# Kernel tuning notes

Measured on AMD Instinct MI355X. Metric: run time of the kernel, lower is better.

Reference implementation:

```python
import jax, jax.numpy as jnp
import numpy as np

B, N, T, CIN = 16, 400, 12, 2
HID, H, D = 256, 8, 32
P, EMB, TOPK, K = 3, 10, 16, 3


def _conv1d(x, w, b, dil):
    # x: (BN, C, T), w: (O, I, K); causal (left) padding like F.pad((pad,0))
    pad = (K - 1) * dil
    y = jax.lax.conv_general_dilated(x, w, (1,), [(pad, 0)], rhs_dilation=(dil,),
                                     dimension_numbers=('NCH', 'OIH', 'NCH'))
    return y + b[None, :, None]


def _ln(x, g, b):
    m = x.mean(-1, keepdims=True)
    v = x.var(-1, keepdims=True)
    return (x - m) / jnp.sqrt(v + 1e-5) * g + b


def setup_inputs() -> dict:
    key = jax.random.key(0)
    kit = iter(jax.random.split(key, 64))

    def g(shape, s=0.05):
        return jax.random.normal(next(kit), shape, jnp.float32) * s

    # fixed graph: ring with 8 neighbors + self loop -> L = 9*N edges
    idx = np.arange(N)
    offs = np.array([-4, -3, -2, -1, 0, 1, 2, 3, 4])
    recv = np.repeat(idx, offs.size)
    send = (recv + np.tile(offs, N)) % N
    L = recv.size

    inp = {
        'x': g((B, N, T, CIN), 1.0),
        'edge_feat': g((B, L, 2), 1.0),
        'fixed_edge_index': jnp.asarray(np.stack([recv, send]).astype(np.int32)),
        # GTCN layer 0 (dilation 1): gate/filter/skip convs + LayerNorm
        'wg0': g((HID, CIN, K)), 'bg0': jnp.zeros((HID,), jnp.float32),
        'wf0': g((HID, CIN, K)), 'bf0': jnp.zeros((HID,), jnp.float32),
        'ws0': g((HID, CIN, K)), 'bs0': jnp.zeros((HID,), jnp.float32),
        'ln0g': jnp.ones((HID,), jnp.float32), 'ln0b': jnp.zeros((HID,), jnp.float32),
        # GTCN layer 1 (dilation 2)
        'wg1': g((HID, HID, K)), 'bg1': jnp.zeros((HID,), jnp.float32),
        'wf1': g((HID, HID, K)), 'bf1': jnp.zeros((HID,), jnp.float32),
        'ws1': g((HID, HID, K)), 'bs1': jnp.zeros((HID,), jnp.float32),
        'ln1g': jnp.ones((HID,), jnp.float32), 'ln1b': jnp.zeros((HID,), jnp.float32),
        'wsk': g((CIN, HID)), 'bsk': jnp.zeros((HID,), jnp.float32),
        # sparse GAT on fixed physical graph (with 2-dim edge features)
        'sWq': g((HID, HID)), 'sWk': g((HID, HID)), 'sWv': g((HID, HID)),
        'sWe': g((2, HID)),
        'saq': g((H, D)), 'sak': g((H, D)), 'sae': g((H, D)),
        # dense GAT on adaptive adjacency
        'dWq': g((HID, HID)), 'dWk': g((HID, HID)), 'dWv': g((HID, HID)),
        'daq': g((H, D)), 'dak': g((H, D)),
        'E1': g((N, EMB), 0.5), 'E2': g((N, EMB), 0.5),
        # gated fusion
        'fW1': g((HID, HID)), 'fb1': jnp.zeros((HID,), jnp.float32),
        'fW2': g((HID, HID)), 'fb2': jnp.zeros((HID,), jnp.float32),
        'fW3': g((HID, HID)), 'fb3': jnp.zeros((HID,), jnp.float32),
        # prediction head
        'Wo': g((HID, P)), 'bo': jnp.zeros((P,), jnp.float32),
    }
    return inp


def reference(x, edge_feat,
              wg0, bg0, wf0, bf0, ws0, bs0, ln0g, ln0b,
              wg1, bg1, wf1, bf1, ws1, bs1, ln1g, ln1b, wsk, bsk,
              sWq, sWk, sWv, sWe, saq, sak, sae,
              dWq, dWk, dWv, daq, dak, E1, E2,
              fW1, fb1, fW2, fb2, fW3, fb3, Wo, bo,
              fixed_edge_index):
    Bb, Nn, Tt, _ = x.shape
    # ---- GTCN (gated temporal conv stack with residual skip) ----
    res = x @ wsk + bsk                                   # (B,N,T,HID)
    xc = x.reshape(Bb * Nn, Tt, -1).transpose(0, 2, 1)    # (BN,C,T)
    for (wg, bg, wf, bf, ws, bs, lg, lb), dil in (
            ((wg0, bg0, wf0, bf0, ws0, bs0, ln0g, ln0b), 1),
            ((wg1, bg1, wf1, bf1, ws1, bs1, ln1g, ln1b), 2)):
        gate = jax.nn.sigmoid(_conv1d(xc, wg, bg, dil))
        y = gate * _conv1d(xc, wf, bf, dil) + (1 - gate) * _conv1d(xc, ws, bs, dil)
        y = jax.nn.relu(_ln(y.transpose(0, 2, 1), lg, lb))  # (BN,T,HID)
        xc = y.transpose(0, 2, 1)
    h = xc.transpose(0, 2, 1).reshape(Bb, Nn, Tt, HID) + res
    hl = h[:, :, -1, :]                                   # (B,N,HID) last step

    # ---- sparse GAT on fixed physical graph (edge features) ----
    recv, send = fixed_edge_index[0], fixed_edge_index[1]
    q = (hl @ sWq).reshape(Bb, Nn, H, D)
    k = (hl @ sWk).reshape(Bb, Nn, H, D)
    v = (hl @ sWv).reshape(Bb, Nn, H, D)
    e = (edge_feat @ sWe).reshape(Bb, -1, H, D)
    s = (q[:, recv] * saq).sum(-1) + (k[:, send] * sak).sum(-1) + (e * sae).sum(-1)
    s = jax.nn.leaky_relu(s, 0.2)                         # (B,L,H)
    mx = jnp.full((Bb, Nn, H), -jnp.inf, s.dtype).at[:, recv].max(s)
    ex = jnp.exp(s - mx[:, recv])
    den = jnp.zeros((Bb, Nn, H), s.dtype).at[:, recv].add(ex)
    alpha = ex / jnp.clip(den[:, recv], 1e-12, None)
    agg = jnp.zeros((Bb, Nn, H, D), v.dtype).at[:, recv].add(alpha[..., None] * v[:, send])
    h_fixed = jax.nn.elu(agg.reshape(Bb, Nn, HID))

    # ---- dense GAT on adaptive (learned, top-k sparsified) adjacency ----
    A = jax.nn.softmax(jax.nn.relu(E1 @ E2.T), axis=-1)   # (N,N)
    kth = jax.lax.top_k(A, TOPK)[0][:, -1:]
    adj_adp = jnp.where(A >= kth, A, 0.0)
    q = (hl @ dWq).reshape(Bb, Nn, H, D)
    k = (hl @ dWk).reshape(Bb, Nn, H, D)
    v = (hl @ dWv).reshape(Bb, Nn, H, D)
    sc = (q * daq).sum(-1)[:, :, None, :] + (k * dak).sum(-1)[:, None, :, :]  # (B,N,N,H)
    sc = jax.nn.leaky_relu(sc, 0.2)
    sc = sc + jnp.log(jnp.clip(adj_adp, 1e-12, None))[None, :, :, None]      # log-adj trick
    sc = jnp.where((adj_adp > 0)[None, :, :, None], sc, -1e9)
    al = jax.nn.softmax(sc, axis=2)
    h_adp = jax.nn.elu(jnp.einsum('bnjh,bjhd->bnhd', al, v).reshape(Bb, Nn, HID))

    # ---- gated fusion + prediction head ----
    gate = jax.nn.sigmoid((h_fixed + h_adp) @ fW1 + fb1)
    fused = jnp.tanh(gate * (h_fixed @ fW2 + fb2) + (1 - gate) * (h_adp @ fW3 + fb3))
    return fused @ Wo + bo                                # (B,N,P)
```

## Files before the change

### kernel.cpp

```cpp
#include <hip/hip_runtime.h>
#include <math.h>

#define LL 3600
#define NODES 6400

typedef __attribute__((ext_vector_type(8))) _Float16 half8;
typedef __attribute__((ext_vector_type(4))) float f32x4;
typedef __attribute__((ext_vector_type(4))) unsigned short ushort4v;

__device__ __forceinline__ unsigned short f2h(float f) {
    union { _Float16 h; unsigned short u; } cv;
    cv.h = (_Float16)f;
    return cv.u;
}
__device__ __forceinline__ float h2f(unsigned short u) {
    union { unsigned short u; _Float16 h; } cv;
    cv.u = u;
    return (float)cv.h;
}

#define GLOAD16(gp, lp) __builtin_amdgcn_global_load_lds( \
    (const __attribute__((address_space(1))) unsigned int*)(const void*)(gp), \
    (__attribute__((address_space(3))) unsigned int*)(void*)(lp), 16, 0, 0)

__global__ __launch_bounds__(256) void prep_kernel(
    const float* __restrict__ wg1, const float* __restrict__ wf1, const float* __restrict__ ws1,
    const float* __restrict__ sWv, const float* __restrict__ dWv,
    const float* __restrict__ sWq, const float* __restrict__ saq,
    const float* __restrict__ sWk, const float* __restrict__ sak,
    const float* __restrict__ dWq, const float* __restrict__ daq,
    const float* __restrict__ dWk, const float* __restrict__ dak,
    const float* __restrict__ fW1, const float* __restrict__ fW2, const float* __restrict__ fW3,
    const float* __restrict__ sWe, const float* __restrict__ sae,
    const float* __restrict__ E1, const float* __restrict__ E2,
    const float* __restrict__ x,
    const float* __restrict__ wg0, const float* __restrict__ bg0,
    const float* __restrict__ wf0, const float* __restrict__ bf0,
    const float* __restrict__ ws0, const float* __restrict__ bs0,
    const float* __restrict__ lg0, const float* __restrict__ lb0,
    const float* __restrict__ bo,
    unsigned short* __restrict__ W1h,
    unsigned short* __restrict__ W2h,
    unsigned short* __restrict__ W3h,
    float* __restrict__ AeS,
    int* __restrict__ cnt, int* __restrict__ idxs, float* __restrict__ logv,
    unsigned short* __restrict__ Xh,
    float* __restrict__ out) {
    int bid = blockIdx.x;
    int tid = threadIdx.x;

    if (bid < 2304) {
        int idx = bid * 256 + tid;
        int n = idx / 768, k = idx % 768;
        int which = n >> 8, o = n & 255;
        int tt = k >> 8, i = k & 255;
        const float* w = which == 0 ? wg1 : (which == 1 ? wf1 : ws1);
        W1h[idx] = f2h(w[(o * 256 + i) * 3 + tt]);
    } else if (bid < 2944) {
        int idx = (bid - 2304) * 256 + tid;
        int n = idx / 256, k = idx % 256;
        float v = 0.f;
        if (n < 256) v = sWv[k * 256 + n];
        else if (n < 512) v = dWv[k * 256 + (n - 256)];
        else if (n < 544) {
            int j = n - 512, g = j >> 3, h = j & 7;
            const float* Wm = g == 0 ? sWq : (g == 1 ? sWk : (g == 2 ? dWq : dWk));
            const float* am = g == 0 ? saq : (g == 1 ? sak : (g == 2 ? daq : dak));
            float s = 0.f;
            for (int d = 0; d < 32; d++) s += Wm[k * 256 + h * 32 + d] * am[h * 32 + d];
            v = s;
        }
        W2h[idx] = f2h(v);
    } else if (bid < 4480) {
        int idx = (bid - 2944) * 256 + tid;
        int n = idx / 512, k = idx % 512;
        float v = 0.f;
        if (k < 256) {
            if (n < 256) v = fW1[k * 256 + n];
            else if (n < 512) v = fW2[k * 256 + (n - 256)];
        } else {
            int c = k - 256;
            if (n < 256) v = fW1[c * 256 + n];
            else if (n >= 512) v = fW3[c * 256 + (n - 512)];
        }
        W3h[idx] = f2h(v);
    } else if (bid == 4480) {
        if (tid < 16) {
            int cc = tid / 8, h = tid % 8;
            float s = 0.f;
            for (int d = 0; d < 32; d++) s += sWe[cc * 256 + h * 32 + d] * sae[h * 32 + d];
            AeS[tid] = s;
        }
    } else if (bid < 4581) {
        int n = ((bid - 4481) * 256 + tid) >> 6;
        int lane = tid & 63;
        if (n >= 400) return;
        float e1[10];
        #pragma unroll
        for (int k = 0; k < 10; k++) e1[k] = E1[n * 10 + k];
        float p[7];
        #pragma unroll
        for (int i = 0; i < 7; i++) {
            int j = i * 64 + lane;
            if (j < 400) {
                float s = 0.f;
                #pragma unroll
                for (int k = 0; k < 10; k++) s += e1[k] * E2[j * 10 + k];
                p[i] = fmaxf(s, 0.f);
            } else p[i] = -1e30f;
        }
        float mx = -1e30f;
        #pragma unroll
        for (int i = 0; i < 7; i++) mx = fmaxf(mx, p[i]);
        #pragma unroll
        for (int o = 32; o > 0; o >>= 1) mx = fmaxf(mx, __shfl_xor(mx, o, 64));
        float sum = 0.f;
        #pragma unroll
        for (int i = 0; i < 7; i++) {
            int j = i * 64 + lane;
            if (j < 400) { p[i] = expf(p[i] - mx); sum += p[i]; }
        }
        #pragma unroll
        for (int o = 32; o > 0; o >>= 1) sum += __shfl_xor(sum, o, 64);
        float inv = 1.f / sum;
        float m[7];
        #pragma unroll
        for (int i = 0; i < 7; i++) {
            int j = i * 64 + lane;
            if (j < 400) { p[i] *= inv; m[i] = p[i]; }
            else m[i] = -1e30f;
        }
        for (int it = 0; it < 15; ++it) {
            float lm = m[0];
            #pragma unroll
            for (int i = 1; i < 7; i++) lm = fmaxf(lm, m[i]);
            float gm = lm;
            #pragma unroll
            for (int o = 32; o > 0; o >>= 1) gm = fmaxf(gm, __shfl_xor(gm, o, 64));
            unsigned long long msk = __ballot(lm == gm);
            int first = (int)(__ffsll((long long)msk)) - 1;
            if (lane == first) {
                #pragma unroll
                for (int i = 0; i < 7; i++) {
                    if (m[i] == gm) { m[i] = -1e30f; break; }
                }
            }
        }
        float kth = m[0];
        #pragma unroll
        for (int i = 1; i < 7; i++) kth = fmaxf(kth, m[i]);
        #pragma unroll
        for (int o = 32; o > 0; o >>= 1) kth = fmaxf(kth, __shfl_xor(kth, o, 64));
        int base = 0;
        #pragma unroll
        for (int i = 0; i < 7; i++) {
            int j = i * 64 + lane;
            bool pred = (j < 400) && (p[i] >= kth);
            unsigned long long msk = __ballot(pred);
            int pre = __popcll(msk & ((lane == 63) ? 0x7fffffffffffffffull : ((1ull << lane) - 1)));
            if (pred) {
                int pos = base + pre;
                if (pos < 64) {
                    idxs[n * 64 + pos] = j;
                    logv[n * 64 + pos] = logf(fmaxf(p[i], 1e-12f));
                }
            }
            base += __popcll(msk);
        }
        if (lane == 0) cnt[n] = base < 64 ? base : 64;
    } else if (bid < 6181) {
        int lane = tid & 63;
        int node = (bid - 4581) * 4 + (tid >> 6);
        float xs[14];
        #pragma unroll
        for (int t = 0; t < 7; t++) {
            xs[t * 2]     = x[(size_t)(node * 12 + 5 + t) * 2];
            xs[t * 2 + 1] = x[(size_t)(node * 12 + 5 + t) * 2 + 1];
        }
        float wg[4][6], wf[4][6], wsv[4][6], bgv[4], bfv[4], bsv[4], gln[4], bln[4];
        #pragma unroll
        for (int cc = 0; cc < 4; cc++) {
            int o = lane * 4 + cc;
            #pragma unroll
            for (int i = 0; i < 6; i++) {
                wg[cc][i] = wg0[o * 6 + i];
                wf[cc][i] = wf0[o * 6 + i];
                wsv[cc][i] = ws0[o * 6 + i];
            }
            bgv[cc] = bg0[o]; bfv[cc] = bf0[o]; bsv[cc] = bs0[o];
            gln[cc] = lg0[o]; bln[cc] = lb0[o];
        }
        #pragma unroll
        for (int tt = 0; tt < 3; tt++) {
            int tb = 2 * tt;
            float y[4];
            float s1 = 0.f, s2 = 0.f;
            #pragma unroll
            for (int cc = 0; cc < 4; cc++) {
                float g = bgv[cc], f = bfv[cc], s = bsv[cc];
                #pragma unroll
                for (int k = 0; k < 3; k++) {
                    #pragma unroll
                    for (int c = 0; c < 2; c++) {
                        float xv = xs[(tb + k) * 2 + c];
                        g += wg[cc][c * 3 + k] * xv;
                        f += wf[cc][c * 3 + k] * xv;
                        s += wsv[cc][c * 3 + k] * xv;
                    }
                }
                float gate = 1.f / (1.f + expf(-g));
                y[cc] = gate * f + (1.f - gate) * s;
                s1 += y[cc];
                s2 += y[cc] * y[cc];
            }
            #pragma unroll
            for (int o = 32; o > 0; o >>= 1) {
                s1 += __shfl_xor(s1, o, 64);
                s2 += __shfl_xor(s2, o, 64);
            }
            float mean = s1 * (1.f / 256.f);
            float var = s2 * (1.f / 256.f) - mean * mean;
            float rstd = rsqrtf(var + 1e-5f);
            unsigned short h4[4];
            #pragma unroll
            for (int cc = 0; cc < 4; cc++) {
                float v = (y[cc] - mean) * rstd * gln[cc] + bln[cc];
                h4[cc] = f2h(fmaxf(v, 0.f));
            }
            unsigned long long pack = (unsigned long long)h4[0] | ((unsigned long long)h4[1] << 16)
                                    | ((unsigned long long)h4[2] << 32) | ((unsigned long long)h4[3] << 48);
            *(unsigned long long*)&Xh[(size_t)node * 768 + tt * 256 + lane * 4] = pack;
        }
    } else {
        int idx = (bid - 6181) * 256 + tid;
        if (idx < NODES * 3) out[idx] = bo[idx % 3];
    }
}

template<int K, int LDC, int GX, int GY>
__global__ __launch_bounds__(256, 3) void gemm_f16_k64(
    const unsigned short* __restrict__ A,
    const unsigned short* __restrict__ BT,
    unsigned short* __restrict__ C) {
    __shared__ __align__(16) unsigned short lA[3][64 * 64];
    __shared__ __align__(16) unsigned short lB[3][64 * 64];
    int tid = threadIdx.x;
    int lane = tid & 63;
    int w = tid >> 6;
    int wm = w >> 1, wn = w & 1;
    int r = lane & 15, g4 = lane >> 4;

    constexpr int NWG = GX * GY;
    constexpr int Q = NWG / 8, R = NWG % 8;
    int flat = blockIdx.y * GX + blockIdx.x;
    int xcd = flat & 7, idx = flat >> 3;
    int nf = (xcd < R ? xcd * (Q + 1) : R * (Q + 1) + (xcd - R) * Q) + idx;
    int col0 = (nf % GX) * 64;
    int row0 = (nf / GX) * 64;

    f32x4 acc[2][2] = {};

    int rA0 = tid >> 3, sl0 = tid & 7;
    int rA1 = 32 + (tid >> 3);
    int tk0 = (sl0 ^ (rA0 & 7)) * 8;
    int tk1 = (sl0 ^ (rA1 & 7)) * 8;

#define STAGE(sel, kk) do { \
    GLOAD16(A + (size_t)(row0 + rA0) * K + (kk) + tk0, &lA[sel][(rA0 * 8 + sl0) * 8]); \
    GLOAD16(A + (size_t)(row0 + rA1) * K + (kk) + tk1, &lA[sel][(rA1 * 8 + sl0) * 8]); \
    GLOAD16(BT + (size_t)(col0 + rA0) * K + (kk) + tk0, &lB[sel][(rA0 * 8 + sl0) * 8]); \
    GLOAD16(BT + (size_t)(col0 + rA1) * K + (kk) + tk1, &lB[sel][(rA1 * 8 + sl0) * 8]); \
} while (0)

#define COMPUTE(cur) do { \
    _Pragma("unroll") \
    for (int ks = 0; ks < 2; ++ks) { \
        int sw = ((ks * 4 + g4) ^ (r & 7)) << 3; \
        half8 a_[2], b_[2]; \
        _Pragma("unroll") \
        for (int mi = 0; mi < 2; ++mi) \
            a_[mi] = *(const half8*)&lA[cur][(wm * 32 + mi * 16 + r) * 64 + sw]; \
        _Pragma("unroll") \
        for (int ni = 0; ni < 2; ++ni) \
            b_[ni] = *(const half8*)&lB[cur][(wn * 32 + ni * 16 + r) * 64 + sw]; \
        _Pragma("unroll") \
        for (int mi = 0; mi < 2; ++mi) \
            _Pragma("unroll") \
            for (int ni = 0; ni < 2; ++ni) \
                acc[mi][ni] = __builtin_amdgcn_mfma_f32_16x16x32_f16(a_[mi], b_[ni], acc[mi][ni], 0, 0, 0); \
    } \
} while (0)

    constexpr int NT = K >> 6;
    STAGE(0, 0);
    STAGE(1, 64);
    for (int t = 0; t < NT - 1; ++t) {
        asm volatile("s_waitcnt vmcnt(4)" ::: "memory");
        __builtin_amdgcn_s_barrier();
        if (t + 2 < NT) STAGE((t + 2) % 3, (t + 2) * 64);
        COMPUTE(t % 3);
    }
    asm volatile("s_waitcnt vmcnt(0)" ::: "memory");
    __builtin_amdgcn_s_barrier();
    COMPUTE((NT - 1) % 3);
#undef STAGE
#undef COMPUTE

    #pragma unroll
    for (int mi = 0; mi < 2; ++mi) {
        #pragma unroll
        for (int ni = 0; ni < 2; ++ni) {
            int rowb = row0 + wm * 32 + mi * 16 + g4 * 4;
            int colb = col0 + wn * 32 + ni * 16 + r;
            #pragma unroll
            for (int j = 0; j < 4; ++j)
                C[(size_t)(rowb + j) * LDC + colb] = f2h(acc[mi][ni][j]);
        }
    }
}

__global__ __launch_bounds__(256, 3) void gemm3_fused(
    const unsigned short* __restrict__ A,
    const unsigned short* __restrict__ BT,
    const float* __restrict__ fb1, const float* __restrict__ fb2, const float* __restrict__ fb3,
    const float* __restrict__ Wo,
    float* __restrict__ out) {
    __shared__ __align__(16) unsigned short lA[3][64 * 32];
    __shared__ __align__(16) unsigned short lB[3][3][64 * 32];
    int tid = threadIdx.x;
    int lane = tid & 63;
    int w = tid >> 6;
    int wm = w >> 1, wn = w & 1;
    int r = lane & 15, g4 = lane >> 4;

    constexpr int NWG = 400;
    constexpr int Q = NWG / 8;
    int flat = blockIdx.y * 4 + blockIdx.x;
    int xcd = flat & 7, idx = flat >> 3;
    int nf = xcd * Q + idx;
    int c0 = (nf % 4) * 64;
    int row0 = (nf / 4) * 64;

    f32x4 acc[3][2][2] = {};

    int rS = tid >> 2;
    int slot = tid & 3;
    int tk = (slot ^ (rS & 3)) * 8;

#define STAGE3(sel, kk) do { \
    GLOAD16(A + (size_t)(row0 + rS) * 512 + (kk) + tk, &lA[sel][tid * 8]); \
    GLOAD16(BT + (size_t)(c0 + rS) * 512 + (kk) + tk, &lB[sel][0][tid * 8]); \
    GLOAD16(BT + (size_t)(c0 + 256 + rS) * 512 + (kk) + tk, &lB[sel][1][tid * 8]); \
    GLOAD16(BT + (size_t)(c0 + 512 + rS) * 512 + (kk) + tk, &lB[sel][2][tid * 8]); \
} while (0)

    int sw = (g4 ^ (r & 3)) << 3;

#define COMPUTE3(cur) do { \
    half8 a_[2], b_[3][2]; \
    _Pragma("unroll") \
    for (int mi = 0; mi < 2; ++mi) \
        a_[mi] = *(const half8*)&lA[cur][(wm * 32 + mi * 16 + r) * 32 + sw]; \
    _Pragma("unroll") \
    for (int q = 0; q < 3; ++q) \
        _Pragma("unroll") \
        for (int ni = 0; ni < 2; ++ni) \
            b_[q][ni] = *(const half8*)&lB[cur][q][(wn * 32 + ni * 16 + r) * 32 + sw]; \
    _Pragma("unroll") \
    for (int q = 0; q < 3; ++q) \
        _Pragma("unroll") \
        for (int mi = 0; mi < 2; ++mi) \
            _Pragma("unroll") \
            for (int ni = 0; ni < 2; ++ni) \
                acc[q][mi][ni] = __builtin_amdgcn_mfma_f32_16x16x32_f16(a_[mi], b_[q][ni], acc[q][mi][ni], 0, 0, 0); \
} while (0)

    constexpr int NT = 16;
    STAGE3(0, 0);
    STAGE3(1, 32);
    for (int t = 0; t < NT - 1; ++t) {
        asm volatile("s_waitcnt vmcnt(4)" ::: "memory");
        __builtin_amdgcn_s_barrier();
        if (t + 2 < NT) STAGE3((t + 2) % 3, (t + 2) * 32);
        COMPUTE3(t % 3);
    }
    asm volatile("s_waitcnt vmcnt(0)" ::: "memory");
    __builtin_amdgcn_s_barrier();
    COMPUTE3((NT - 1) % 3);
#undef STAGE3
#undef COMPUTE3

    #pragma unroll
    for (int mi = 0; mi < 2; ++mi) {
        float v0[4] = {}, v1[4] = {}, v2[4] = {};
        #pragma unroll
        for (int ni = 0; ni < 2; ++ni) {
            int ch = c0 + wn * 32 + ni * 16 + r;
            float b1 = fb1[ch], b2 = fb2[ch], b3 = fb3[ch];
            float w0 = Wo[ch * 3 + 0], w1 = Wo[ch * 3 + 1], w2 = Wo[ch * 3 + 2];
            #pragma unroll
            for (int j = 0; j < 4; ++j) {
                float g = 1.f / (1.f + expf(-(acc[0][mi][ni][j] + b1)));
                float a2 = acc[1][mi][ni][j] + b2;
                float a3 = acc[2][mi][ni][j] + b3;
                float fused = tanhf(g * a2 + (1.f - g) * a3);
                v0[j] += fused * w0;
                v1[j] += fused * w1;
                v2[j] += fused * w2;
            }
        }
        #pragma unroll
        for (int off = 1; off < 16; off <<= 1) {
            #pragma unroll
            for (int j = 0; j < 4; ++j) {
                v0[j] += __shfl_xor(v0[j], off, 64);
                v1[j] += __shfl_xor(v1[j], off, 64);
                v2[j] += __shfl_xor(v2[j], off, 64);
            }
        }
        if (r == 0) {
            int rowb = row0 + wm * 32 + mi * 16 + g4 * 4;
            #pragma unroll
            for (int j = 0; j < 4; ++j) {
                atomicAdd(&out[(size_t)(rowb + j) * 3 + 0], v0[j]);
                atomicAdd(&out[(size_t)(rowb + j) * 3 + 1], v1[j]);
                atomicAdd(&out[(size_t)(rowb + j) * 3 + 2], v2[j]);
            }
        }
    }
}

__global__ __launch_bounds__(256) void epi1_kernel(
    const unsigned short* __restrict__ Y1, const float* __restrict__ x,
    const float* __restrict__ bg1, const float* __restrict__ bf1, const float* __restrict__ bs1,
    const float* __restrict__ lg, const float* __restrict__ lb,
    const float* __restrict__ wsk, const float* __restrict__ bsk,
    unsigned short* __restrict__ HLh) {
    int lane = threadIdx.x & 63;
    int node = blockIdx.x * 4 + (threadIdx.x >> 6);
    size_t base = (size_t)node * 768;
    ushort4v yg = *(const ushort4v*)&Y1[base + lane * 4];
    ushort4v yf = *(const ushort4v*)&Y1[base + 256 + lane * 4];
    ushort4v ys = *(const ushort4v*)&Y1[base + 512 + lane * 4];
    float y[4];
    float s1 = 0.f, s2 = 0.f;
    #pragma unroll
    for (int cc = 0; cc < 4; cc++) {
        int o = lane * 4 + cc;
        float g = h2f(yg[cc]) + bg1[o];
        float f = h2f(yf[cc]) + bf1[o];
        float s = h2f(ys[cc]) + bs1[o];
        float gate = 1.f / (1.f + expf(-g));
        y[cc] = gate * f + (1.f - gate) * s;
        s1 += y[cc];
        s2 += y[cc] * y[cc];
    }
    #pragma unroll
    for (int off = 32; off > 0; off >>= 1) {
        s1 += __shfl_xor(s1, off, 64);
        s2 += __shfl_xor(s2, off, 64);
    }
    float mean = s1 * (1.f / 256.f);
    float var = s2 * (1.f / 256.f) - mean * mean;
    float rstd = rsqrtf(var + 1e-5f);
    float x0 = x[(size_t)(node * 12 + 11) * 2];
    float x1 = x[(size_t)(node * 12 + 11) * 2 + 1];
    unsigned short h4[4];
    #pragma unroll
    for (int cc = 0; cc < 4; cc++) {
        int o = lane * 4 + cc;
        float v = (y[cc] - mean) * rstd * lg[o] + lb[o];
        v = fmaxf(v, 0.f);
        float res = x0 * wsk[o] + x1 * wsk[256 + o] + bsk[o];
        h4[cc] = f2h(v + res);
    }
    unsigned long long pack = (unsigned long long)h4[0] | ((unsigned long long)h4[1] << 16)
                            | ((unsigned long long)h4[2] << 32) | ((unsigned long long)h4[3] << 48);
    *(unsigned long long*)&HLh[(size_t)node * 256 + lane * 4] = pack;
}

__global__ __launch_bounds__(256) void gat_kernel(
    const unsigned short* __restrict__ Y2, const float* __restrict__ ef,
    const int* __restrict__ fei, const float* __restrict__ AeS,
    const int* __restrict__ cnt, const int* __restrict__ idxs, const float* __restrict__ logv,
    unsigned short* __restrict__ Uh) {
    int node = (blockIdx.x & 7) * 800 + (blockIdx.x >> 3);
    int b = node / 400, n = node % 400;
    int tid = threadIdx.x;
    __shared__ int snd[9];
    __shared__ float alf[9][8];
    __shared__ float invdf[8];
    __shared__ int jidx[64];
    __shared__ float sca[64][8];
    __shared__ float alb[64][8];
    __shared__ float invda[8];
    __shared__ float svf[9][8];
    int c = cnt[n];

    if (tid < 64) {
        int lane = tid;
        if (lane < 9) snd[lane] = fei[LL + n * 9 + lane];
        for (int e = lane; e < 72; e += 64) {
            int j = e >> 3, h = e & 7;
            int l = n * 9 + j;
            float e0 = ef[((size_t)b * LL + l) * 2];
            float e1 = ef[((size_t)b * LL + l) * 2 + 1];
            float ae = e0 * AeS[h] + e1 * AeS[8 + h];
            float aq = h2f(Y2[(size_t)node * 640 + 512 + h]);
            float ak = h2f(Y2[((size_t)(b * 400 + snd[j])) * 640 + 520 + h]);
            float s = aq + ak + ae;
            svf[j][h] = s > 0.f ? s : 0.2f * s;
        }
        if (lane < 8) {
            int h = lane;
            float mx = -1e30f;
            #pragma unroll
            for (int j = 0; j < 9; j++) mx = fmaxf(mx, svf[j][h]);
            float den = 0.f;
            #pragma unroll
            for (int j = 0; j < 9; j++) { float e = expf(svf[j][h] - mx); alf[j][h] = e; den += e; }
            invdf[h] = 1.f / fmaxf(den, 1e-12f);
        }
    } else if (tid < 128) {
        int lane = tid - 64;
        if (lane < c) jidx[lane] = idxs[n * 64 + lane];
        float jl = (lane < c) ? logv[n * 64 + lane] : 0.f;
        for (int e = lane; e < c * 8; e += 64) {
            int j = e >> 3, h = e & 7;
            float aq = h2f(Y2[(size_t)node * 640 + 528 + h]);
            float ak = h2f(Y2[((size_t)(b * 400 + jidx[j])) * 640 + 536 + h]);
            float s = aq + ak;
            s = s > 0.f ? s : 0.2f * s;
            sca[j][h] = s + __shfl(jl, j, 64);
        }
        int h = lane >> 3, grp = lane & 7;
        float mx = -1e30f;
        for (int j = grp; j < c; j += 8) mx = fmaxf(mx, sca[j][h]);
        #pragma unroll
        for (int o = 1; o < 8; o <<= 1) mx = fmaxf(mx, __shfl_xor(mx, o, 64));
        float s = 0.f;
        for (int j = grp; j < c; j += 8) { float e = expf(sca[j][h] - mx); alb[j][h] = e; s += e; }
        #pragma unroll
        for (int o = 1; o < 8; o <<= 1) s += __shfl_xor(s, o, 64);
        if (grp == 0) invda[h] = 1.f / s;
    }
    __syncthreads();

    if (tid < 128) {
        int ch = tid * 2;
        int h = ch >> 5;
        float a0 = 0.f, a1 = 0.f;
        #pragma unroll
        for (int j = 0; j < 9; j++) {
            unsigned v = *(const unsigned*)&Y2[((size_t)(b * 400 + snd[j])) * 640 + ch];
            float al = alf[j][h];
            a0 += al * h2f((unsigned short)(v & 0xffff));
            a1 += al * h2f((unsigned short)(v >> 16));
        }
        float iv = invdf[h];
        a0 *= iv; a1 *= iv;
        a0 = a0 > 0.f ? a0 : (expf(a0) - 1.f);
        a1 = a1 > 0.f ? a1 : (expf(a1) - 1.f);
        unsigned o = (unsigned)f2h(a0) | ((unsigned)f2h(a1) << 16);
        *(unsigned*)&Uh[(size_t)node * 512 + ch] = o;
    } else {
        int ch = (tid - 128) * 2;
        int h = ch >> 5;
        float p0a = 0.f, p0b = 0.f, p1a = 0.f, p1b = 0.f;
        float p2a = 0.f, p2b = 0.f, p3a = 0.f, p3b = 0.f;
        int j = 0;
        for (; j + 4 <= c; j += 4) {
            unsigned v0 = *(const unsigned*)&Y2[((size_t)(b * 400 + jidx[j])) * 640 + 256 + ch];
            unsigned v1 = *(const unsigned*)&Y2[((size_t)(b * 400 + jidx[j + 1])) * 640 + 256 + ch];
            unsigned v2 = *(const unsigned*)&Y2[((size_t)(b * 400 + jidx[j + 2])) * 640 + 256 + ch];
            unsigned v3 = *(const unsigned*)&Y2[((size_t)(b * 400 + jidx[j + 3])) * 640 + 256 + ch];
            float l0 = alb[j][h], l1 = alb[j + 1][h], l2 = alb[j + 2][h], l3 = alb[j + 3][h];
            p0a += l0 * h2f((unsigned short)(v0 & 0xffff));
            p0b += l0 * h2f((unsigned short)(v0 >> 16));
            p1a += l1 * h2f((unsigned short)(v1 & 0xffff));
            p1b += l1 * h2f((unsigned short)(v1 >> 16));
            p2a += l2 * h2f((unsigned short)(v2 & 0xffff));
            p2b += l2 * h2f((unsigned short)(v2 >> 16));
            p3a += l3 * h2f((unsigned short)(v3 & 0xffff));
            p3b += l3 * h2f((unsigned short)(v3 >> 16));
        }
        for (; j < c; j++) {
            unsigned v = *(const unsigned*)&Y2[((size_t)(b * 400 + jidx[j])) * 640 + 256 + ch];
            float al = alb[j][h];
            p0a += al * h2f((unsigned short)(v & 0xffff));
            p0b += al * h2f((unsigned short)(v >> 16));
        }
        float a0 = (p0a + p1a) + (p2a + p3a);
        float a1 = (p0b + p1b) + (p2b + p3b);
        float iv = invda[h];
        a0 *= iv; a1 *= iv;
        a0 = a0 > 0.f ? a0 : (expf(a0) - 1.f);
        a1 = a1 > 0.f ? a1 : (expf(a1) - 1.f);
        unsigned o = (unsigned)f2h(a0) | ((unsigned)f2h(a1) << 16);
        *(unsigned*)&Uh[(size_t)node * 512 + 256 + ch] = o;
    }
}

extern "C" void kernel_launch(void* const* d_in, const int* in_sizes, int n_in,
                              void* d_out, int out_size, void* d_ws, size_t ws_size,
                              hipStream_t stream) {
    const float* x   = (const float*)d_in[0];
    const float* ef  = (const float*)d_in[1];
    const int*   fei = (const int*)d_in[2];
    const float* wg0 = (const float*)d_in[3];
    const float* bg0 = (const float*)d_in[4];
    const float* wf0 = (const float*)d_in[5];
    const float* bf0 = (const float*)d_in[6];
    const float* ws0 = (const float*)d_in[7];
    const float* bs0 = (const float*)d_in[8];
    const float* ln0g = (const float*)d_in[9];
    const float* ln0b = (const float*)d_in[10];
    const float* wg1 = (const float*)d_in[11];
    const float* bg1 = (const float*)d_in[12];
    const float* wf1 = (const float*)d_in[13];
    const float* bf1 = (const float*)d_in[14];
    const float* ws1 = (const float*)d_in[15];
    const float* bs1 = (const float*)d_in[16];
    const float* ln1g = (const float*)d_in[17];
    const float* ln1b = (const float*)d_in[18];
    const float* wsk = (const float*)d_in[19];
    const float* bsk = (const float*)d_in[20];
    const float* sWq = (const float*)d_in[21];
    const float* sWk = (const float*)d_in[22];
    const float* sWv = (const float*)d_in[23];
    const float* sWe = (const float*)d_in[24];
    const float* saq = (const float*)d_in[25];
    const float* sak = (const float*)d_in[26];
    const float* sae = (const float*)d_in[27];
    const float* dWq = (const float*)d_in[28];
    const float* dWk = (const float*)d_in[29];
    const float* dWv = (const float*)d_in[30];
    const float* daq = (const float*)d_in[31];
    const float* dak = (const float*)d_in[32];
    const float* E1  = (const float*)d_in[33];
    const float* E2  = (const float*)d_in[34];
    const float* fW1 = (const float*)d_in[35];
    const float* fb1 = (const float*)d_in[36];
    const float* fW2 = (const float*)d_in[37];
    const float* fb2 = (const float*)d_in[38];
    const float* fW3 = (const float*)d_in[39];
    const float* fb3 = (const float*)d_in[40];
    const float* Wo  = (const float*)d_in[41];
    const float* bo  = (const float*)d_in[42];
    float* out = (float*)d_out;

    char* b = (char*)d_ws;
    unsigned short* Xh  = (unsigned short*)(b + 0);
    unsigned short* Yh  = (unsigned short*)(b + 9830400);
    unsigned short* HLh = (unsigned short*)(b + 19660800);
    unsigned short* Uh  = (unsigned short*)(b + 22937600);
    unsigned short* W1h = (unsigned short*)(b + 29491200);
    unsigned short* W2h = (unsigned short*)(b + 30670848);
    unsigned short* W3h = (unsigned short*)(b + 30998528);
    float*          AES = (float*)(b + 31784960);
    float*          LOGV= (float*)(b + 31785216);
    int*            CNT = (int*)(b + 31887616);
    int*            IDX = (int*)(b + 31889216);

    prep_kernel<<<6256, 256, 0, stream>>>(
        wg1, wf1, ws1,
        sWv, dWv, sWq, saq, sWk, sak, dWq, daq, dWk, dak,
        fW1, fW2, fW3, sWe, sae, E1, E2,
        x, wg0, bg0, wf0, bf0, ws0, bs0, ln0g, ln0b, bo,
        W1h, W2h, W3h, AES,
        CNT, IDX, LOGV, Xh, out);

    gemm_f16_k64<768, 768, 12, 100><<<dim3(12, 100), 256, 0, stream>>>(Xh, W1h, Yh);

    epi1_kernel<<<1600, 256, 0, stream>>>(Yh, x, bg1, bf1, bs1, ln1g, ln1b, wsk, bsk, HLh);

    gemm_f16_k64<256, 640, 9, 100><<<dim3(9, 100), 256, 0, stream>>>(HLh, W2h, Yh);

    gat_kernel<<<NODES, 256, 0, stream>>>(Yh, ef, fei, AES, CNT, IDX, LOGV, Uh);

    gemm3_fused<<<dim3(4, 100), 256, 0, stream>>>(Uh, W3h, fb1, fb2, fb3, Wo, out);
}
```

Baseline: 92.97 us.

## Fuse gated-TCN epilogue and LayerNorm into the second GEMM prologue

Removes the separate epilogue kernel by computing the gate, LayerNorm, ReLU and residual for each 64-row tile inside the second GEMM, writing the fp16 A tile directly to shared memory. This drops one launch and the intermediate activation write and read. In exchange every column-tile block recomputes the epilogue for its rows, re-reading the three 256-wide Y1 slices once per column tile, and each thread holds 64 floats in registers. The output moves to a new workspace buffer.

```diff
diff --git a/kernel.cpp b/kernel.cpp
--- a/kernel.cpp
+++ b/kernel.cpp
@@ -319,6 +319,124 @@
     }
 }
 
+__global__ __launch_bounds__(256, 2) void gemm2_fused(
+    const unsigned short* __restrict__ Y1, const float* __restrict__ x,
+    const float* __restrict__ bg1, const float* __restrict__ bf1, const float* __restrict__ bs1,
+    const float* __restrict__ lg, const float* __restrict__ lb,
+    const float* __restrict__ wsk, const float* __restrict__ bsk,
+    const unsigned short* __restrict__ BT,
+    unsigned short* __restrict__ C) {
+    __shared__ __align__(16) unsigned short hl[4][64 * 64];
+    __shared__ __align__(16) unsigned short lB[4][64 * 64];
+    int tid = threadIdx.x;
+    int lane = tid & 63;
+    int w = tid >> 6;
+    int wm = w >> 1, wn = w & 1;
+    int r = lane & 15, g4 = lane >> 4;
+
+    constexpr int NWG = 900, Q = NWG / 8, RR = NWG % 8;
+    int flat = blockIdx.y * 9 + blockIdx.x;
+    int xcd = flat & 7, idx = flat >> 3;
+    int nf = (xcd < RR ? xcd * (Q + 1) : RR * (Q + 1) + (xcd - RR) * Q) + idx;
+    int col0 = (nf % 9) * 64;
+    int row0 = (nf / 9) * 64;
+
+    {
+        int ra = tid >> 3, sl = tid & 7;
+        int rb = 32 + ra;
+        int tka = (sl ^ (ra & 7)) * 8;
+        int tkb = (sl ^ (rb & 7)) * 8;
+        #pragma unroll
+        for (int kt = 0; kt < 4; ++kt) {
+            GLOAD16(BT + (size_t)(col0 + ra) * 256 + kt * 64 + tka, &lB[kt][tid * 8]);
+            GLOAD16(BT + (size_t)(col0 + rb) * 256 + kt * 64 + tkb, &lB[kt][2048 + tid * 8]);
+        }
+    }
+
+    int row = tid >> 2, kt = tid & 3;
+    int node = row0 + row;
+    int ob = kt * 64;
+    float y[64];
+    float s1 = 0.f, s2 = 0.f;
+    {
+        size_t base = (size_t)node * 768 + ob;
+        #pragma unroll
+        for (int g = 0; g < 8; ++g) {
+            half8 vg = *(const half8*)&Y1[base + g * 8];
+            half8 vf = *(const half8*)&Y1[base + 256 + g * 8];
+            half8 vs = *(const half8*)&Y1[base + 512 + g * 8];
+            #pragma unroll
+            for (int e = 0; e < 8; ++e) {
+                int o = ob + g * 8 + e;
+                float gg = (float)vg[e] + bg1[o];
+                float ff = (float)vf[e] + bf1[o];
+                float ss = (float)vs[e] + bs1[o];
+                float gate = 1.f / (1.f + expf(-gg));
+                float yy = gate * ff + (1.f - gate) * ss;
+                y[g * 8 + e] = yy;
+                s1 += yy;
+                s2 += yy * yy;
+            }
+        }
+    }
+    s1 += __shfl_xor(s1, 1, 64); s2 += __shfl_xor(s2, 1, 64);
+    s1 += __shfl_xor(s1, 2, 64); s2 += __shfl_xor(s2, 2, 64);
+    float mean = s1 * (1.f / 256.f);
+    float var = s2 * (1.f / 256.f) - mean * mean;
+    float rstd = rsqrtf(var + 1e-5f);
+    float x0 = x[(size_t)(node * 12 + 11) * 2];
+    float x1 = x[(size_t)(node * 12 + 11) * 2 + 1];
+    #pragma unroll
+    for (int s = 0; s < 8; ++s) {
+        half8 hv;
+        #pragma unroll
+        for (int e = 0; e < 8; ++e) {
+            int o = ob + s * 8 + e;
+            float v = (y[s * 8 + e] - mean) * rstd * lg[o] + lb[o];
+            v = fmaxf(v, 0.f);
+            float res = x0 * wsk[o] + x1 * wsk[256 + o] + bsk[o];
+            hv[e] = (_Float16)(v + res);
+        }
+        *(half8*)&hl[kt][row * 64 + ((s ^ (row & 7)) * 8)] = hv;
+    }
+
+    asm volatile("s_waitcnt vmcnt(0)" ::: "memory");
+    __syncthreads();
+
+    f32x4 acc[2][2] = {};
+    #pragma unroll
+    for (int ktt = 0; ktt < 4; ++ktt) {
+        #pragma unroll
+        for (int ks = 0; ks < 2; ++ks) {
+            int sw = ((ks * 4 + g4) ^ (r & 7)) << 3;
+            half8 a_[2], b_[2];
+            #pragma unroll
+            for (int mi = 0; mi < 2; ++mi)
+                a_[mi] = *(const half8*)&hl[ktt][(wm * 32 + mi * 16 + r) * 64 + sw];
+            #pragma unroll
+            for (int ni = 0; ni < 2; ++ni)
+                b_[ni] = *(const half8*)&lB[ktt][(wn * 32 + ni * 16 + r) * 64 + sw];
+            #pragma unroll
+            for (int mi = 0; mi < 2; ++mi)
+                #pragma unroll
+                for (int ni = 0; ni < 2; ++ni)
+                    acc[mi][ni] = __builtin_amdgcn_mfma_f32_16x16x32_f16(a_[mi], b_[ni], acc[mi][ni], 0, 0, 0);
+        }
+    }
+
+    #pragma unroll
+    for (int mi = 0; mi < 2; ++mi) {
+        #pragma unroll
+        for (int ni = 0; ni < 2; ++ni) {
+            int rowb = row0 + wm * 32 + mi * 16 + g4 * 4;
+            int colb = col0 + wn * 32 + ni * 16 + r;
+            #pragma unroll
+            for (int j = 0; j < 4; ++j)
+                C[(size_t)(rowb + j) * 640 + colb] = f2h(acc[mi][ni][j]);
+        }
+    }
+}
+
 __global__ __launch_bounds__(256, 3) void gemm3_fused(
     const unsigned short* __restrict__ A,
     const unsigned short* __restrict__ BT,
@@ -428,55 +546,6 @@
             }
         }
     }
-}
-
-__global__ __launch_bounds__(256) void epi1_kernel(
-    const unsigned short* __restrict__ Y1, const float* __restrict__ x,
-    const float* __restrict__ bg1, const float* __restrict__ bf1, const float* __restrict__ bs1,
-    const float* __restrict__ lg, const float* __restrict__ lb,
-    const float* __restrict__ wsk, const float* __restrict__ bsk,
-    unsigned short* __restrict__ HLh) {
-    int lane = threadIdx.x & 63;
-    int node = blockIdx.x * 4 + (threadIdx.x >> 6);
-    size_t base = (size_t)node * 768;
-    ushort4v yg = *(const ushort4v*)&Y1[base + lane * 4];
-    ushort4v yf = *(const ushort4v*)&Y1[base + 256 + lane * 4];
-    ushort4v ys = *(const ushort4v*)&Y1[base + 512 + lane * 4];
-    float y[4];
-    float s1 = 0.f, s2 = 0.f;
-    #pragma unroll
-    for (int cc = 0; cc < 4; cc++) {
-        int o = lane * 4 + cc;
-        float g = h2f(yg[cc]) + bg1[o];
-        float f = h2f(yf[cc]) + bf1[o];
-        float s = h2f(ys[cc]) + bs1[o];
-        float gate = 1.f / (1.f + expf(-g));
-        y[cc] = gate * f + (1.f - gate) * s;
-        s1 += y[cc];
-        s2 += y[cc] * y[cc];
-    }
-    #pragma unroll
-    for (int off = 32; off > 0; off >>= 1) {
-        s1 += __shfl_xor(s1, off, 64);
-        s2 += __shfl_xor(s2, off, 64);
-    }
-    float mean = s1 * (1.f / 256.f);
-    float var = s2 * (1.f / 256.f) - mean * mean;
-    float rstd = rsqrtf(var + 1e-5f);
-    float x0 = x[(size_t)(node * 12 + 11) * 2];
-    float x1 = x[(size_t)(node * 12 + 11) * 2 + 1];
-    unsigned short h4[4];
-    #pragma unroll
-    for (int cc = 0; cc < 4; cc++) {
-        int o = lane * 4 + cc;
-        float v = (y[cc] - mean) * rstd * lg[o] + lb[o];
-        v = fmaxf(v, 0.f);
-        float res = x0 * wsk[o] + x1 * wsk[256 + o] + bsk[o];
-        h4[cc] = f2h(v + res);
-    }
-    unsigned long long pack = (unsigned long long)h4[0] | ((unsigned long long)h4[1] << 16)
-                            | ((unsigned long long)h4[2] << 32) | ((unsigned long long)h4[3] << 48);
-    *(unsigned long long*)&HLh[(size_t)node * 256 + lane * 4] = pack;
 }
 
 __global__ __launch_bounds__(256) void gat_kernel(
@@ -652,15 +721,15 @@
     char* b = (char*)d_ws;
     unsigned short* Xh  = (unsigned short*)(b + 0);
     unsigned short* Yh  = (unsigned short*)(b + 9830400);
-    unsigned short* HLh = (unsigned short*)(b + 19660800);
-    unsigned short* Uh  = (unsigned short*)(b + 22937600);
-    unsigned short* W1h = (unsigned short*)(b + 29491200);
-    unsigned short* W2h = (unsigned short*)(b + 30670848);
-    unsigned short* W3h = (unsigned short*)(b + 30998528);
-    float*          AES = (float*)(b + 31784960);
-    float*          LOGV= (float*)(b + 31785216);
-    int*            CNT = (int*)(b + 31887616);
-    int*            IDX = (int*)(b + 31889216);
+    unsigned short* Y2h = (unsigned short*)(b + 19660800);
+    unsigned short* Uh  = (unsigned short*)(b + 27852800);
+    unsigned short* W1h = (unsigned short*)(b + 34406400);
+    unsigned short* W2h = (unsigned short*)(b + 35586048);
+    unsigned short* W3h = (unsigned short*)(b + 35913728);
+    float*          AES = (float*)(b + 36700160);
+    float*          LOGV= (float*)(b + 36700416);
+    int*            CNT = (int*)(b + 36802816);
+    int*            IDX = (int*)(b + 36804416);
 
     prep_kernel<<<6256, 256, 0, stream>>>(
         wg1, wf1, ws1,
@@ -672,11 +741,9 @@
 
     gemm_f16_k64<768, 768, 12, 100><<<dim3(12, 100), 256, 0, stream>>>(Xh, W1h, Yh);
 
-    epi1_kernel<<<1600, 256, 0, stream>>>(Yh, x, bg1, bf1, bs1, ln1g, ln1b, wsk, bsk, HLh);
-
-    gemm_f16_k64<256, 640, 9, 100><<<dim3(9, 100), 256, 0, stream>>>(HLh, W2h, Yh);
-
-    gat_kernel<<<NODES, 256, 0, stream>>>(Yh, ef, fei, AES, CNT, IDX, LOGV, Uh);
+    gemm2_fused<<<dim3(9, 100), 256, 0, stream>>>(Yh, x, bg1, bf1, bs1, ln1g, ln1b, wsk, bsk, W2h, Y2h);
+
+    gat_kernel<<<NODES, 256, 0, stream>>>(Y2h, ef, fei, AES, CNT, IDX, LOGV, Uh);
 
     gemm3_fused<<<dim3(4, 100), 256, 0, stream>>>(Uh, W3h, fb1, fb2, fb3, Wo, out);
 }
```

Result: slower. 150.4 us (+61.8%).
